# Kernel tuning notes

Hardware: AMD Instinct MI355X
Metric: run time of the kernel (lower is better)

Reference implementation:

```python
import jax, jax.numpy as jnp
import numpy as np

NEG_SLOPE = 0.2

def gat_layer(x, src, dst, W, b, a_src, a_dst, heads, out_dim, concat):
    N = x.shape[0]
    h = (x @ W).reshape(N, heads, out_dim)            # [N,H,D]
    s_src = jnp.sum(h * a_src, axis=-1)               # [N,H]
    s_dst = jnp.sum(h * a_dst, axis=-1)               # [N,H]
    e = jax.nn.leaky_relu(s_src[src] + s_dst[dst], NEG_SLOPE)  # [E,H]
    # segment softmax over destination nodes (self-loops guarantee nonempty segments)
    m = jax.ops.segment_max(e, dst, num_segments=N)
    e = jnp.exp(e - m[dst])
    denom = jax.ops.segment_sum(e, dst, num_segments=N)
    alpha = e / denom[dst]                            # [E,H]
    msg = h[src] * alpha[:, :, None]                  # [E,H,D]
    out = jax.ops.segment_sum(msg, dst, num_segments=N)  # [N,H,D]
    if concat:
        out = out.reshape(N, heads * out_dim)
    else:
        out = out.mean(axis=1)
    return out + b

def setup_inputs() -> dict:
    key = jax.random.key(0)
    ks = jax.random.split(key, 16)
    N, E = 50000, 1600000
    IN, HID, OUT, H = 128, 256, 32, 4
    D = HID // H
    def glorot(k, shape):
        fan = shape[0] + shape[-1]
        return jax.random.uniform(k, shape, jnp.float32, -1.0, 1.0) * np.sqrt(6.0 / fan)
    x = jax.random.normal(ks[0], (N, IN), jnp.float32)
    edge_index = jax.random.randint(ks[1], (2, E), 0, N, jnp.int32)
    return {
        "x": x, "edge_index": edge_index,
        "W0": glorot(ks[2], (IN, H * D)), "b0": jnp.zeros((H * D,), jnp.float32),
        "asrc0": glorot(ks[3], (H, D)), "adst0": glorot(ks[4], (H, D)),
        "W1": glorot(ks[5], (HID, H * D)), "b1": jnp.zeros((H * D,), jnp.float32),
        "asrc1": glorot(ks[6], (H, D)), "adst1": glorot(ks[7], (H, D)),
        "W2": glorot(ks[8], (HID, 1 * OUT)), "b2": jnp.zeros((OUT,), jnp.float32),
        "asrc2": glorot(ks[9], (1, OUT)), "adst2": glorot(ks[10], (1, OUT)),
    }

def reference(x, edge_index, W0, b0, asrc0, adst0, W1, b1, asrc1, adst1, W2, b2, asrc2, adst2):
    N = x.shape[0]
    # add self-loops (PyG GATConv default)
    loop = jnp.arange(N, dtype=edge_index.dtype)
    src = jnp.concatenate([edge_index[0], loop])
    dst = jnp.concatenate([edge_index[1], loop])
    h = gat_layer(x, src, dst, W0, b0, asrc0, adst0, heads=4, out_dim=64, concat=True)
    h = jax.nn.elu(h)
    h = gat_layer(h, src, dst, W1, b1, asrc1, adst1, heads=4, out_dim=64, concat=True)
    h = jax.nn.elu(h)
    h = gat_layer(h, src, dst, W2, b2, asrc2, adst2, heads=1, out_dim=32, concat=False)
    return jax.nn.log_softmax(h, axis=1)
```

## Files before the change

kernel.cpp:

```cpp
#include <hip/hip_runtime.h>
#include <hip/hip_bf16.h>
#include <math.h>

#define IN_DIM 128
#define HID    256
#define OUTD   32
#define HEADS  4
#define NB_SH  7
#define BUCKET_CAP 6144
#define NCHUNK_BLKS 256

typedef __attribute__((ext_vector_type(8))) short s8v;
typedef __attribute__((ext_vector_type(4))) float f4v;

__device__ inline unsigned short f2bf(float f) {
    union { __hip_bfloat16 b; unsigned short u; } cv;
    cv.b = __float2bfloat16(f);
    return cv.u;
}


__global__ __launch_bounds__(256) void csr_hist(const int* __restrict__ ei,
                                                int* __restrict__ H,
                                                int E, int N, int NB, int per_blk) {
    __shared__ int hist[512];
    int t = threadIdx.x;
    for (int i = t; i < NB; i += 256) hist[i] = 0;
    __syncthreads();
    int lo = blockIdx.x * per_blk;
    int hi = min(lo + per_blk, E + N);
    for (int e = lo + t; e < hi; e += 256) {
        int dst = (e < E) ? ei[E + e] : (e - E);
        atomicAdd(&hist[dst >> NB_SH], 1);
    }
    __syncthreads();
    for (int i = t; i < NB; i += 256) H[blockIdx.x * NB + i] = hist[i];
}

__global__ __launch_bounds__(256) void csr_colscan(int* __restrict__ H,
                                                   int* __restrict__ total, int NB) {
    int b = blockIdx.x, t = threadIdx.x;
    int v = H[t * NB + b];
    __shared__ int s[256];
    s[t] = v;
    __syncthreads();
    for (int o = 1; o < 256; o <<= 1) {
        int x = (t >= o) ? s[t - o] : 0;
        __syncthreads();
        s[t] += x;
        __syncthreads();
    }
    H[t * NB + b] = s[t] - v;
    if (t == 255) total[b] = s[255];
}

__global__ void csr_basescan(const int* __restrict__ total, int* __restrict__ base, int NB) {
    __shared__ int s[512];
    int t = threadIdx.x;
    int v = (t < NB) ? total[t] : 0;
    s[t] = v;
    __syncthreads();
    for (int o = 1; o < 512; o <<= 1) {
        int x = (t >= o) ? s[t - o] : 0;
        __syncthreads();
        s[t] += x;
        __syncthreads();
    }
    if (t < NB) base[t] = s[t] - v;
    if (t == NB - 1) base[NB] = s[t];
}

__global__ __launch_bounds__(256) void csr_partition(const int* __restrict__ ei,
                                                     const int* __restrict__ H,
                                                     const int* __restrict__ base,
                                                     int* __restrict__ ebuf,
                                                     int E, int N, int per_blk, int NB) {
    __shared__ int cur[512];
    int t = threadIdx.x;
    for (int i = t; i < NB; i += 256) cur[i] = base[i] + H[blockIdx.x * NB + i];
    __syncthreads();
    int lo = blockIdx.x * per_blk;
    int hi = min(lo + per_blk, E + N);
    for (int e = lo + t; e < hi; e += 256) {
        int src = (e < E) ? ei[e] : (e - E);
        int dst = (e < E) ? ei[E + e] : (e - E);
        int pos = atomicAdd(&cur[dst >> NB_SH], 1);
        ebuf[pos] = src | ((dst & 127) << 16);
    }
}

__global__ __launch_bounds__(256) void csr_sort(const int* __restrict__ ebuf,
                                                const int* __restrict__ base,
                                                int* __restrict__ col,
                                                int* __restrict__ rp, int N, int NB) {
    int b = blockIdx.x, t = threadIdx.x;
    int lo = base[b], hi = base[b + 1];
    int nbase = b << NB_SH;
    __shared__ int c_[128], sc[128], cur[128];
    __shared__ int loc[BUCKET_CAP];
    if (t < 128) c_[t] = 0;
    __syncthreads();
    for (int k = lo + t; k < hi; k += 256) atomicAdd(&c_[(ebuf[k] >> 16) & 127], 1);
    __syncthreads();
    if (t < 128) sc[t] = c_[t];
    __syncthreads();
    for (int o = 1; o < 128; o <<= 1) {
        int x = 0;
        if (t < 128 && t >= o) x = sc[t - o];
        __syncthreads();
        if (t < 128) sc[t] += x;
        __syncthreads();
    }
    if (t < 128) {
        int excl = sc[t] - c_[t];
        cur[t] = excl;
        int node = nbase + t;
        if (node < N) rp[node] = lo + excl;
    }
    if (b == NB - 1 && t == 0) rp[N] = hi;
    __syncthreads();
    for (int k = lo + t; k < hi; k += 256) {
        int e = ebuf[k];
        int p = atomicAdd(&cur[(e >> 16) & 127], 1);
        if (p < BUCKET_CAP) loc[p] = e & 0xFFFF;
    }
    __syncthreads();
    int m = min(hi - lo, BUCKET_CAP);
    for (int k = t; k < m; k += 256) col[lo + k] = loc[k];
}


__global__ __launch_bounds__(256) void prep_w(const float* __restrict__ W,
                                              unsigned short* __restrict__ Wt_h,
                                              unsigned short* __restrict__ Wt_l,
                                              int K, int N) {
    int idx = blockIdx.x * 256 + threadIdx.x;
    if (idx >= K * N) return;
    int n = idx / K, k = idx % K;
    float x = W[(size_t)k * N + n];
    unsigned short h = f2bf(x);
    float hf = __uint_as_float((unsigned)h << 16);
    Wt_h[idx] = h;
    Wt_l[idx] = f2bf(x - hf);
}


template <int BN>
__global__ __launch_bounds__(256, 2) void gemm_mfma(const float* __restrict__ A,
                                                    const unsigned short* __restrict__ Wt_h,
                                                    const unsigned short* __restrict__ Wt_l,
                                                    unsigned short* __restrict__ Cb,
                                                    const float* __restrict__ asrc,
                                                    const float* __restrict__ adst,
                                                    float* __restrict__ ssrcO,
                                                    float* __restrict__ sdstO,
                                                    int M, int K, int Nst, int Hn) {
    constexpr int WROWS = (BN == 128) ? 64 : 32;
    constexpr int WCOLS = (BN == 128) ? 64 : 32;
    constexpr int MI = WROWS / 16, NJ = WCOLS / 16;
    __shared__ unsigned short As_h[128][64], As_l[128][64];
    __shared__ unsigned short Bs_h[BN][64], Bs_l[BN][64];
    int tid = threadIdx.x;
    int lane = tid & 63, w = tid >> 6;
    int wm, wn;
    if (BN == 128) { wm = w & 1; wn = w >> 1; } else { wm = w; wn = 0; }
    int row0 = blockIdx.x * 128, col0 = blockIdx.y * BN;

    f4v acc[MI][NJ];
#pragma unroll
    for (int i = 0; i < MI; i++)
#pragma unroll
        for (int j = 0; j < NJ; j++) acc[i][j] = (f4v)(0.f);

    for (int k0 = 0; k0 < K; k0 += 64) {
#pragma unroll
        for (int i = 0; i < 4; i++) {
            int c = tid + i * 256;
            int r = c >> 3, ch = c & 7;
            int grow = row0 + r;
            float x[8];
            if (grow < M) {
                float4 v0 = *(const float4*)(A + (size_t)grow * K + k0 + ch * 8);
                float4 v1 = *(const float4*)(A + (size_t)grow * K + k0 + ch * 8 + 4);
                x[0] = v0.x; x[1] = v0.y; x[2] = v0.z; x[3] = v0.w;
                x[4] = v1.x; x[5] = v1.y; x[6] = v1.z; x[7] = v1.w;
            } else {
#pragma unroll
                for (int j = 0; j < 8; j++) x[j] = 0.f;
            }
            union { unsigned short u[8]; uint4 q; } hu, lu;
#pragma unroll
            for (int j = 0; j < 8; j++) {
                hu.u[j] = f2bf(x[j]);
                float hf = __uint_as_float((unsigned)hu.u[j] << 16);
                lu.u[j] = f2bf(x[j] - hf);
            }
            int chs = ch ^ (r & 7);
            *(uint4*)&As_h[r][chs * 8] = hu.q;
            *(uint4*)&As_l[r][chs * 8] = lu.q;
        }
#pragma unroll
        for (int i = 0; i < BN * 8 / 256; i++) {
            int c = tid + i * 256;
            int n = c >> 3, ch = c & 7;
            int chs = ch ^ (n & 7);
            size_t g = (size_t)(col0 + n) * K + k0 + ch * 8;
            *(uint4*)&Bs_h[n][chs * 8] = *(const uint4*)(Wt_h + g);
            *(uint4*)&Bs_l[n][chs * 8] = *(const uint4*)(Wt_l + g);
        }
        __syncthreads();
#pragma unroll
        for (int ks = 0; ks < 2; ks++) {
            s8v ah[MI], al[MI], bh[NJ], bl[NJ];
            int kc = ks * 4 + (lane >> 4);
            int lr = lane & 15;
#pragma unroll
            for (int i = 0; i < MI; i++) {
                int r = wm * WROWS + i * 16 + lr;
                ah[i] = *(const s8v*)&As_h[r][(kc ^ (r & 7)) * 8];
                al[i] = *(const s8v*)&As_l[r][(kc ^ (r & 7)) * 8];
            }
#pragma unroll
            for (int j = 0; j < NJ; j++) {
                int n = wn * WCOLS + j * 16 + lr;
                bh[j] = *(const s8v*)&Bs_h[n][(kc ^ (n & 7)) * 8];
                bl[j] = *(const s8v*)&Bs_l[n][(kc ^ (n & 7)) * 8];
            }
#pragma unroll
            for (int i = 0; i < MI; i++)
#pragma unroll
                for (int j = 0; j < NJ; j++) {
                    acc[i][j] = __builtin_amdgcn_mfma_f32_16x16x32_bf16(ah[i], bh[j], acc[i][j], 0, 0, 0);
                    acc[i][j] = __builtin_amdgcn_mfma_f32_16x16x32_bf16(ah[i], bl[j], acc[i][j], 0, 0, 0);
                    acc[i][j] = __builtin_amdgcn_mfma_f32_16x16x32_bf16(al[i], bh[j], acc[i][j], 0, 0, 0);
                }
        }
        __syncthreads();
    }
    int lr = lane & 15, lg = lane >> 4;
#pragma unroll
    for (int i = 0; i < MI; i++)
#pragma unroll
        for (int j = 0; j < NJ; j++) {
            int gcol = col0 + wn * WCOLS + j * 16 + lr;
#pragma unroll
            for (int rr = 0; rr < 4; rr++) {
                int grow = row0 + wm * WROWS + i * 16 + lg * 4 + rr;
                if (grow < M) Cb[(size_t)grow * Nst + gcol] = f2bf(acc[i][j][rr]);
            }
        }
    int hd = (BN == 128) ? (blockIdx.y * 2 + wn) : 0;
    float as_[NJ], ad_[NJ];
#pragma unroll
    for (int j = 0; j < NJ; j++) {
        int gcol = col0 + wn * WCOLS + j * 16 + lr;
        as_[j] = asrc[gcol];
        ad_[j] = adst[gcol];
    }
#pragma unroll
    for (int i = 0; i < MI; i++)
#pragma unroll
        for (int rr = 0; rr < 4; rr++) {
            float ps = 0.f, pd = 0.f;
#pragma unroll
            for (int j = 0; j < NJ; j++) {
                ps += acc[i][j][rr] * as_[j];
                pd += acc[i][j][rr] * ad_[j];
            }
#pragma unroll
            for (int off = 1; off < 16; off <<= 1) {
                ps += __shfl_xor(ps, off);
                pd += __shfl_xor(pd, off);
            }
            int grow = row0 + wm * WROWS + i * 16 + lg * 4 + rr;
            if (lr == 0 && grow < M) {
                ssrcO[(size_t)grow * Hn + hd] = ps;
                sdstO[(size_t)grow * Hn + hd] = pd;
            }
        }
}


template <int CH, int H, int MODE>
__global__ __launch_bounds__(256) void gat_fused(const unsigned short* __restrict__ hb,
                                                 const float* __restrict__ ssrc,
                                                 const float* __restrict__ sdst,
                                                 const int* __restrict__ rp,
                                                 const int* __restrict__ col,
                                                 const float* __restrict__ bias,
                                                 float* __restrict__ out, int N) {
    const int TPE = CH / 8;
    const int EPW = 64 / TPE;
    const int D = CH / H;
    int wv = threadIdx.x >> 6, lane = threadIdx.x & 63;
    int n = blockIdx.x * 4 + wv;
    if (n >= N) return;
    int k0 = __builtin_amdgcn_readfirstlane(rp[n]);
    int k1 = __builtin_amdgcn_readfirstlane(rp[n + 1]);

    int h1 = lane % H;
    int slot = lane / H;
    const int SL = 64 / H;
    float sd1 = sdst[(size_t)n * H + h1];
    float m = -1e30f, l = 0.f;
    for (int k = k0 + slot; k < k1; k += SL) {
        int s = col[k];
        float e = ssrc[(size_t)s * H + h1] + sd1;
        e = (e > 0.f) ? e : 0.2f * e;
        float mn = fmaxf(m, e);
        l = l * __expf(m - mn) + __expf(e - mn);
        m = mn;
    }
#pragma unroll
    for (int off = H; off < 64; off <<= 1) {
        float m2 = __shfl_xor(m, off);
        float l2 = __shfl_xor(l, off);
        float mn = fmaxf(m, m2);
        l = l * __expf(m - mn) + l2 * __expf(m2 - mn);
        m = mn;
    }

    int eo = lane / TPE;
    int c = (lane % TPE) * 8;
    int head = c / D;
    float mh = __shfl(m, head);
    float invl = 1.f / __shfl(l, head);
    float sdh = __shfl(sd1, head);

    float acc[8];
#pragma unroll
    for (int j = 0; j < 8; j++) acc[j] = 0.f;

    for (int k = k0; k < k1; k += 4 * EPW) {
        int ss[4];
        float aa[4];
#pragma unroll
        for (int u = 0; u < 4; u++) {
            int ku = k + u * EPW + eo;
            bool v = ku < k1;
            ss[u] = col[v ? ku : k0];
            aa[u] = v ? invl : 0.f;
        }
#pragma unroll
        for (int u = 0; u < 4; u++) {
            float e = ssrc[(size_t)ss[u] * H + head] + sdh;
            e = (e > 0.f) ? e : 0.2f * e;
            aa[u] *= __expf(e - mh);
        }
        uint4 hv[4];
#pragma unroll
        for (int u = 0; u < 4; u++) hv[u] = *(const uint4*)(hb + (size_t)ss[u] * CH + c);
#pragma unroll
        for (int u = 0; u < 4; u++) {
            const unsigned* p = (const unsigned*)&hv[u];
#pragma unroll
            for (int q = 0; q < 4; q++) {
                acc[2 * q]     += aa[u] * __uint_as_float(p[q] << 16);
                acc[2 * q + 1] += aa[u] * __uint_as_float(p[q] & 0xffff0000u);
            }
        }
    }
#pragma unroll
    for (int off = TPE; off < 64; off <<= 1)
#pragma unroll
        for (int j = 0; j < 8; j++) acc[j] += __shfl_xor(acc[j], off);
    if (eo != 0) return;
    float o[8];
#pragma unroll
    for (int j = 0; j < 8; j++) o[j] = acc[j] + bias[c + j];
    if (MODE == 0) {
#pragma unroll
        for (int j = 0; j < 8; j++) o[j] = (o[j] > 0.f) ? o[j] : expm1f(o[j]);
    } else {
        float mx = o[0];
#pragma unroll
        for (int j = 1; j < 8; j++) mx = fmaxf(mx, o[j]);
#pragma unroll
        for (int off = 1; off < TPE; off <<= 1) mx = fmaxf(mx, __shfl_xor(mx, off));
        float sm = 0.f;
#pragma unroll
        for (int j = 0; j < 8; j++) sm += __expf(o[j] - mx);
#pragma unroll
        for (int off = 1; off < TPE; off <<= 1) sm += __shfl_xor(sm, off);
        float lg = logf(sm) + mx;
#pragma unroll
        for (int j = 0; j < 8; j++) o[j] -= lg;
    }
    float4* op = (float4*)(out + (size_t)n * CH + c);
    op[0] = make_float4(o[0], o[1], o[2], o[3]);
    op[1] = make_float4(o[4], o[5], o[6], o[7]);
}


extern "C" void kernel_launch(void* const* d_in, const int* in_sizes, int n_in,
                              void* d_out, int out_size, void* d_ws, size_t ws_size,
                              hipStream_t stream) {
    const float* x   = (const float*)d_in[0];
    const int*   ei  = (const int*)d_in[1];
    const float* W0  = (const float*)d_in[2];
    const float* b0  = (const float*)d_in[3];
    const float* as0 = (const float*)d_in[4];
    const float* ad0 = (const float*)d_in[5];
    const float* W1  = (const float*)d_in[6];
    const float* b1  = (const float*)d_in[7];
    const float* as1 = (const float*)d_in[8];
    const float* ad1 = (const float*)d_in[9];
    const float* W2  = (const float*)d_in[10];
    const float* b2  = (const float*)d_in[11];
    const float* as2 = (const float*)d_in[12];
    const float* ad2 = (const float*)d_in[13];

    int N = in_sizes[0] / IN_DIM;
    int E = in_sizes[1] / 2;
    int Et = E + N;
    int NB = (N + 127) >> NB_SH;

    char* w = (char*)d_ws;
    size_t off = 0;
    auto alloc = [&](size_t bytes) -> void* {
        void* p = w + off;
        off = (off + bytes + 255) & ~(size_t)255;
        return p;
    };
    float*          Q     = (float*)alloc((size_t)N * HID * 4);
    unsigned short* Ab    = (unsigned short*)alloc((size_t)N * HID * 2);
    float*          ssrc  = (float*)alloc((size_t)N * HEADS * 4);
    float*          sdst  = (float*)alloc((size_t)N * HEADS * 4);
    int*            rp    = (int*)alloc((size_t)(N + 1) * 4);
    int*            col   = (int*)alloc((size_t)Et * 4);
    int*            H     = (int*)alloc((size_t)NCHUNK_BLKS * NB * 4);
    int*            total = (int*)alloc((size_t)(NB + 1) * 4);
    int*            base  = (int*)alloc((size_t)(NB + 1) * 4);
    int*            ebuf  = (int*)alloc((size_t)Et * 4);
    unsigned short* Wt0h  = (unsigned short*)alloc((size_t)IN_DIM * HID * 2);
    unsigned short* Wt0l  = (unsigned short*)alloc((size_t)IN_DIM * HID * 2);
    unsigned short* Wt1h  = (unsigned short*)alloc((size_t)HID * HID * 2);
    unsigned short* Wt1l  = (unsigned short*)alloc((size_t)HID * HID * 2);
    unsigned short* Wt2h  = (unsigned short*)alloc((size_t)HID * OUTD * 2);
    unsigned short* Wt2l  = (unsigned short*)alloc((size_t)HID * OUTD * 2);

    prep_w<<<(IN_DIM * HID + 255) / 256, 256, 0, stream>>>(W0, Wt0h, Wt0l, IN_DIM, HID);
    prep_w<<<(HID * HID + 255) / 256, 256, 0, stream>>>(W1, Wt1h, Wt1l, HID, HID);
    prep_w<<<(HID * OUTD + 255) / 256, 256, 0, stream>>>(W2, Wt2h, Wt2l, HID, OUTD);

    int per_blk = (Et + NCHUNK_BLKS - 1) / NCHUNK_BLKS;
    csr_hist<<<NCHUNK_BLKS, 256, 0, stream>>>(ei, H, E, N, NB, per_blk);
    csr_colscan<<<NB, 256, 0, stream>>>(H, total, NB);
    csr_basescan<<<1, 512, 0, stream>>>(total, base, NB);
    csr_partition<<<NCHUNK_BLKS, 256, 0, stream>>>(ei, H, base, ebuf, E, N, per_blk, NB);
    csr_sort<<<NB, 256, 0, stream>>>(ebuf, base, col, rp, N, NB);

    dim3 gm((N + 127) / 128, 2);
    dim3 gm2((N + 127) / 128, 1);
    int gg = (N + 3) / 4;

    gemm_mfma<128><<<gm, 256, 0, stream>>>(x, Wt0h, Wt0l, Ab, as0, ad0, ssrc, sdst,
                                           N, IN_DIM, HID, HEADS);
    gat_fused<HID, HEADS, 0><<<gg, 256, 0, stream>>>(Ab, ssrc, sdst, rp, col, b0, Q, N);

    gemm_mfma<128><<<gm, 256, 0, stream>>>(Q, Wt1h, Wt1l, Ab, as1, ad1, ssrc, sdst,
                                           N, HID, HID, HEADS);
    gat_fused<HID, HEADS, 0><<<gg, 256, 0, stream>>>(Ab, ssrc, sdst, rp, col, b1, Q, N);

    gemm_mfma<32><<<gm2, 256, 0, stream>>>(Q, Wt2h, Wt2l, Ab, as2, ad2, ssrc, sdst,
                                           N, HID, OUTD, 1);
    gat_fused<OUTD, 1, 1><<<gg, 256, 0, stream>>>(Ab, ssrc, sdst, rp, col, b2,
                                                  (float*)d_out, N);
}
```

Baseline: 422.1 us.

## Emit bf16 hi/lo split activations from aggregation, retune gather unroll

The aggregation kernel now writes its ELU output directly as bf16 high/low pairs, and the input features are pre-split by a new prep_x kernel. The GEMM therefore loads ready-made bf16 tiles instead of converting fp32 per tile. The gather loop gets a templated unroll factor (6 for the hidden layers, 2 for the last) with shift-based addressing, and feature loads are issued before the score loads. The goal is to cut conversion ALU work in the GEMM and raise memory-level parallelism in the gathers. The cost is an extra pass over x and an extra intermediate buffer.

```diff
diff --git a/kernel.cpp b/kernel.cpp
--- a/kernel.cpp
+++ b/kernel.cpp
@@ -144,9 +144,30 @@
     Wt_l[idx] = f2bf(x - hf);
 }
 
+__global__ __launch_bounds__(256) void prep_x(const float* __restrict__ X,
+                                              unsigned short* __restrict__ Xh,
+                                              unsigned short* __restrict__ Xl,
+                                              int total8) {
+    int idx = blockIdx.x * 256 + threadIdx.x;
+    if (idx >= total8) return;
+    size_t b = (size_t)idx * 8;
+    float4 v0 = *(const float4*)(X + b);
+    float4 v1 = *(const float4*)(X + b + 4);
+    float x[8] = {v0.x, v0.y, v0.z, v0.w, v1.x, v1.y, v1.z, v1.w};
+    union { unsigned short s[8]; uint4 q; } h, l;
+#pragma unroll
+    for (int j = 0; j < 8; j++) {
+        h.s[j] = f2bf(x[j]);
+        l.s[j] = f2bf(x[j] - __uint_as_float((unsigned)h.s[j] << 16));
+    }
+    *(uint4*)(Xh + b) = h.q;
+    *(uint4*)(Xl + b) = l.q;
+}
+
 
 template <int BN>
-__global__ __launch_bounds__(256, 2) void gemm_mfma(const float* __restrict__ A,
+__global__ __launch_bounds__(256, 2) void gemm_mfma(const unsigned short* __restrict__ Ah,
+                                                    const unsigned short* __restrict__ Al,
                                                     const unsigned short* __restrict__ Wt_h,
                                                     const unsigned short* __restrict__ Wt_l,
                                                     unsigned short* __restrict__ Cb,
@@ -175,34 +196,23 @@
     for (int k0 = 0; k0 < K; k0 += 64) {
 #pragma unroll
         for (int i = 0; i < 4; i++) {
-            int c = tid + i * 256;
-            int r = c >> 3, ch = c & 7;
+            int cidx = tid + i * 256;
+            int r = cidx >> 3, ch = cidx & 7;
             int grow = row0 + r;
-            float x[8];
+            uint4 vh = make_uint4(0, 0, 0, 0), vl = make_uint4(0, 0, 0, 0);
             if (grow < M) {
-                float4 v0 = *(const float4*)(A + (size_t)grow * K + k0 + ch * 8);
-                float4 v1 = *(const float4*)(A + (size_t)grow * K + k0 + ch * 8 + 4);
-                x[0] = v0.x; x[1] = v0.y; x[2] = v0.z; x[3] = v0.w;
-                x[4] = v1.x; x[5] = v1.y; x[6] = v1.z; x[7] = v1.w;
-            } else {
-#pragma unroll
-                for (int j = 0; j < 8; j++) x[j] = 0.f;
-            }
-            union { unsigned short u[8]; uint4 q; } hu, lu;
-#pragma unroll
-            for (int j = 0; j < 8; j++) {
-                hu.u[j] = f2bf(x[j]);
-                float hf = __uint_as_float((unsigned)hu.u[j] << 16);
-                lu.u[j] = f2bf(x[j] - hf);
+                size_t g = (size_t)grow * K + k0 + ch * 8;
+                vh = *(const uint4*)(Ah + g);
+                vl = *(const uint4*)(Al + g);
             }
             int chs = ch ^ (r & 7);
-            *(uint4*)&As_h[r][chs * 8] = hu.q;
-            *(uint4*)&As_l[r][chs * 8] = lu.q;
+            *(uint4*)&As_h[r][chs * 8] = vh;
+            *(uint4*)&As_l[r][chs * 8] = vl;
         }
 #pragma unroll
         for (int i = 0; i < BN * 8 / 256; i++) {
-            int c = tid + i * 256;
-            int n = c >> 3, ch = c & 7;
+            int cidx = tid + i * 256;
+            int n = cidx >> 3, ch = cidx & 7;
             int chs = ch ^ (n & 7);
             size_t g = (size_t)(col0 + n) * K + k0 + ch * 8;
             *(uint4*)&Bs_h[n][chs * 8] = *(const uint4*)(Wt_h + g);
@@ -281,17 +291,21 @@
 }
 
 
-template <int CH, int H, int MODE>
+template <int CH, int H, int MODE, int UNR>
 __global__ __launch_bounds__(256) void gat_fused(const unsigned short* __restrict__ hb,
                                                  const float* __restrict__ ssrc,
                                                  const float* __restrict__ sdst,
                                                  const int* __restrict__ rp,
                                                  const int* __restrict__ col,
                                                  const float* __restrict__ bias,
-                                                 float* __restrict__ out, int N) {
+                                                 float* __restrict__ outF,
+                                                 unsigned short* __restrict__ outH,
+                                                 unsigned short* __restrict__ outL, int N) {
     const int TPE = CH / 8;
     const int EPW = 64 / TPE;
     const int D = CH / H;
+    constexpr int SHCH = (CH == 256) ? 9 : 6;
+    constexpr int SHS = (H == 4) ? 4 : 2;
     int wv = threadIdx.x >> 6, lane = threadIdx.x & 63;
     int n = blockIdx.x * 4 + wv;
     if (n >= N) return;
@@ -327,31 +341,37 @@
     float invl = 1.f / __shfl(l, head);
     float sdh = __shfl(sd1, head);
 
+    const char* hbc = (const char*)hb;
+    const char* ssc = (const char*)ssrc;
+    unsigned cb = (unsigned)(c << 1);
+    unsigned hb4 = (unsigned)(head << 2);
+
     float acc[8];
 #pragma unroll
     for (int j = 0; j < 8; j++) acc[j] = 0.f;
 
-    for (int k = k0; k < k1; k += 4 * EPW) {
-        int ss[4];
-        float aa[4];
-#pragma unroll
-        for (int u = 0; u < 4; u++) {
+    for (int k = k0; k < k1; k += UNR * EPW) {
+        int ss[UNR];
+        float aa[UNR];
+#pragma unroll
+        for (int u = 0; u < UNR; u++) {
             int ku = k + u * EPW + eo;
             bool v = ku < k1;
             ss[u] = col[v ? ku : k0];
             aa[u] = v ? invl : 0.f;
         }
-#pragma unroll
-        for (int u = 0; u < 4; u++) {
-            float e = ssrc[(size_t)ss[u] * H + head] + sdh;
+        uint4 hv[UNR];
+#pragma unroll
+        for (int u = 0; u < UNR; u++)
+            hv[u] = *(const uint4*)(hbc + (((unsigned)ss[u] << SHCH) + cb));
+#pragma unroll
+        for (int u = 0; u < UNR; u++) {
+            float e = *(const float*)(ssc + (((unsigned)ss[u] << SHS) + hb4)) + sdh;
             e = (e > 0.f) ? e : 0.2f * e;
             aa[u] *= __expf(e - mh);
         }
-        uint4 hv[4];
-#pragma unroll
-        for (int u = 0; u < 4; u++) hv[u] = *(const uint4*)(hb + (size_t)ss[u] * CH + c);
-#pragma unroll
-        for (int u = 0; u < 4; u++) {
+#pragma unroll
+        for (int u = 0; u < UNR; u++) {
             const unsigned* p = (const unsigned*)&hv[u];
 #pragma unroll
             for (int q = 0; q < 4; q++) {
@@ -364,14 +384,11 @@
     for (int off = TPE; off < 64; off <<= 1)
 #pragma unroll
         for (int j = 0; j < 8; j++) acc[j] += __shfl_xor(acc[j], off);
-    if (eo != 0) return;
+
     float o[8];
 #pragma unroll
     for (int j = 0; j < 8; j++) o[j] = acc[j] + bias[c + j];
-    if (MODE == 0) {
-#pragma unroll
-        for (int j = 0; j < 8; j++) o[j] = (o[j] > 0.f) ? o[j] : expm1f(o[j]);
-    } else {
+    if (MODE == 1) {
         float mx = o[0];
 #pragma unroll
         for (int j = 1; j < 8; j++) mx = fmaxf(mx, o[j]);
@@ -383,12 +400,22 @@
 #pragma unroll
         for (int off = 1; off < TPE; off <<= 1) sm += __shfl_xor(sm, off);
         float lg = logf(sm) + mx;
-#pragma unroll
-        for (int j = 0; j < 8; j++) o[j] -= lg;
-    }
-    float4* op = (float4*)(out + (size_t)n * CH + c);
-    op[0] = make_float4(o[0], o[1], o[2], o[3]);
-    op[1] = make_float4(o[4], o[5], o[6], o[7]);
+        if (eo != 0) return;
+        float4* op = (float4*)(outF + (size_t)n * CH + c);
+        op[0] = make_float4(o[0] - lg, o[1] - lg, o[2] - lg, o[3] - lg);
+        op[1] = make_float4(o[4] - lg, o[5] - lg, o[6] - lg, o[7] - lg);
+    } else {
+        if (eo != 0) return;
+        union { unsigned short s[8]; uint4 q; } ph, pl;
+#pragma unroll
+        for (int j = 0; j < 8; j++) {
+            float v = (o[j] > 0.f) ? o[j] : expm1f(o[j]);
+            ph.s[j] = f2bf(v);
+            pl.s[j] = f2bf(v - __uint_as_float((unsigned)ph.s[j] << 16));
+        }
+        *(uint4*)(outH + (size_t)n * CH + c) = ph.q;
+        *(uint4*)(outL + (size_t)n * CH + c) = pl.q;
+    }
 }
 
 
@@ -422,8 +449,11 @@
         off = (off + bytes + 255) & ~(size_t)255;
         return p;
     };
-    float*          Q     = (float*)alloc((size_t)N * HID * 4);
+    unsigned short* Qh    = (unsigned short*)alloc((size_t)N * HID * 2);
+    unsigned short* Ql    = (unsigned short*)alloc((size_t)N * HID * 2);
     unsigned short* Ab    = (unsigned short*)alloc((size_t)N * HID * 2);
+    unsigned short* xh    = (unsigned short*)alloc((size_t)N * IN_DIM * 2);
+    unsigned short* xl    = (unsigned short*)alloc((size_t)N * IN_DIM * 2);
     float*          ssrc  = (float*)alloc((size_t)N * HEADS * 4);
     float*          sdst  = (float*)alloc((size_t)N * HEADS * 4);
     int*            rp    = (int*)alloc((size_t)(N + 1) * 4);
@@ -442,6 +472,8 @@
     prep_w<<<(IN_DIM * HID + 255) / 256, 256, 0, stream>>>(W0, Wt0h, Wt0l, IN_DIM, HID);
     prep_w<<<(HID * HID + 255) / 256, 256, 0, stream>>>(W1, Wt1h, Wt1l, HID, HID);
     prep_w<<<(HID * OUTD + 255) / 256, 256, 0, stream>>>(W2, Wt2h, Wt2l, HID, OUTD);
+    int t8 = N * IN_DIM / 8;
+    prep_x<<<(t8 + 255) / 256, 256, 0, stream>>>(x, xh, xl, t8);
 
     int per_blk = (Et + NCHUNK_BLKS - 1) / NCHUNK_BLKS;
     csr_hist<<<NCHUNK_BLKS, 256, 0, stream>>>(ei, H, E, N, NB, per_blk);
@@ -454,16 +486,18 @@
     dim3 gm2((N + 127) / 128, 1);
     int gg = (N + 3) / 4;
 
-    gemm_mfma<128><<<gm, 256, 0, stream>>>(x, Wt0h, Wt0l, Ab, as0, ad0, ssrc, sdst,
+    gemm_mfma<128><<<gm, 256, 0, stream>>>(xh, xl, Wt0h, Wt0l, Ab, as0, ad0, ssrc, sdst,
                                            N, IN_DIM, HID, HEADS);
-    gat_fused<HID, HEADS, 0><<<gg, 256, 0, stream>>>(Ab, ssrc, sdst, rp, col, b0, Q, N);
-
-    gemm_mfma<128><<<gm, 256, 0, stream>>>(Q, Wt1h, Wt1l, Ab, as1, ad1, ssrc, sdst,
+    gat_fused<HID, HEADS, 0, 6><<<gg, 256, 0, stream>>>(Ab, ssrc, sdst, rp, col, b0,
+                                                        nullptr, Qh, Ql, N);
+
+    gemm_mfma<128><<<gm, 256, 0, stream>>>(Qh, Ql, Wt1h, Wt1l, Ab, as1, ad1, ssrc, sdst,
                                            N, HID, HID, HEADS);
-    gat_fused<HID, HEADS, 0><<<gg, 256, 0, stream>>>(Ab, ssrc, sdst, rp, col, b1, Q, N);
-
-    gemm_mfma<32><<<gm2, 256, 0, stream>>>(Q, Wt2h, Wt2l, Ab, as2, ad2, ssrc, sdst,
+    gat_fused<HID, HEADS, 0, 6><<<gg, 256, 0, stream>>>(Ab, ssrc, sdst, rp, col, b1,
+                                                        nullptr, Qh, Ql, N);
+
+    gemm_mfma<32><<<gm2, 256, 0, stream>>>(Qh, Ql, Wt2h, Wt2l, Ab, as2, ad2, ssrc, sdst,
                                            N, HID, OUTD, 1);
-    gat_fused<OUTD, 1, 1><<<gg, 256, 0, stream>>>(Ab, ssrc, sdst, rp, col, b2,
-                                                  (float*)d_out, N);
-}
+    gat_fused<OUTD, 1, 1, 2><<<gg, 256, 0, stream>>>(Ab, ssrc, sdst, rp, col, b2,
+                                                     (float*)d_out, nullptr, nullptr, N);
+}
```

Measured after the change: 430.3 us. No clear change (+1.9%).
